# Performance work log

Hardware: AMD Instinct MI355X
Metric: run time of the kernel (lower is better)

## Reference

```python
import jax, jax.numpy as jnp
import numpy as np

HEADS = 16
NEG_INF = np.float32(-2**32 + 1)  # matches TF code's padding value


def setup_inputs() -> dict:
    key = jax.random.key(0)
    ks = jax.random.split(key, 11)
    B, S, D = 2, 2048, 1024
    mk = lambda k, shape: jax.random.normal(k, shape, dtype=jnp.float32)
    return {
        "query": mk(ks[0], (B, S, D)),
        "key":   mk(ks[1], (B, S, D)),
        "value": mk(ks[2], (B, S, D)),
        "Wq": mk(ks[3], (D, D)) * (1.0 / np.sqrt(D)), "bq": jnp.zeros((D,), jnp.float32),
        "Wk": mk(ks[4], (D, D)) * (1.0 / np.sqrt(D)), "bk": jnp.zeros((D,), jnp.float32),
        "Wv": mk(ks[5], (D, D)) * (1.0 / np.sqrt(D)), "bv": jnp.zeros((D,), jnp.float32),
        "Wo": mk(ks[6], (D, D)) * (1.0 / np.sqrt(D)), "bo": jnp.zeros((D,), jnp.float32),
    }


def reference(query, key, value, Wq, bq, Wk, bk, Wv, bv, Wo, bo):
    B, S, D = query.shape
    H = HEADS
    dh = D // H
    # QKV projections with relu (as in the original Dense(activation=relu))
    q = jax.nn.relu(query @ Wq + bq).reshape(B, S, H, dh)
    k = jax.nn.relu(key   @ Wk + bk).reshape(B, S, H, dh)
    v = jax.nn.relu(value @ Wv + bv).reshape(B, S, H, dh)
    # scaled dot-product attention; scale = sqrt(per-head key dim)
    scores = jnp.einsum("bqhd,bkhd->bhqk", q, k) / jnp.sqrt(jnp.float32(dh))
    # causal mask (masked=True path): zeros above the diagonal -> NEG_INF
    causal = jnp.tril(jnp.ones((S, S), dtype=jnp.float32))  # [S,S]
    scores = jnp.where(causal == 0, NEG_INF, scores)
    attn = jax.nn.softmax(scores, axis=-1)  # [B,H,S,S]
    out = jnp.einsum("bhqk,bkhd->bqhd", attn, v).reshape(B, S, D)
    return jax.nn.relu(out @ Wo + bo)
```

## Files before the change

### kernel.cpp

```cpp
#include <hip/hip_runtime.h>
#include <hip/hip_bf16.h>

using bf16 = __hip_bfloat16;
typedef __attribute__((ext_vector_type(8))) short bf16x8;
typedef __attribute__((ext_vector_type(4))) float f32x4;

#define DEV __device__ __forceinline__

DEV void gload_lds16(const void* g, void* l) {
  __builtin_amdgcn_global_load_lds((const __attribute__((address_space(1))) void*)g,
                                   (__attribute__((address_space(3))) void*)l, 16, 0, 0);
}

DEV unsigned pk2(float lo, float hi) {
  union { bf16 h[2]; unsigned u; } z;
  z.h[0] = __float2bfloat16(lo);
  z.h[1] = __float2bfloat16(hi);
  return z.u;
}

struct PrepArgs {
  const float* x[3]; bf16* y[3];
  const float* W[4]; bf16* WT[4];
};

__global__ __launch_bounds__(256) void prep_kernel(PrepArgs a) {
  __shared__ float tile[32][33];
  const int b = blockIdx.x;
  if (b < 6144) {
    const int which = b >> 11, blk = b & 2047;
    const int i = blk * 256 + threadIdx.x;
    const float4* xv = (const float4*)a.x[which];
    float4 p = xv[i * 2];
    float4 q = xv[i * 2 + 1];
    union { bf16 h[8]; uint4 v; } u;
    u.h[0] = __float2bfloat16(p.x); u.h[1] = __float2bfloat16(p.y);
    u.h[2] = __float2bfloat16(p.z); u.h[3] = __float2bfloat16(p.w);
    u.h[4] = __float2bfloat16(q.x); u.h[5] = __float2bfloat16(q.y);
    u.h[6] = __float2bfloat16(q.z); u.h[7] = __float2bfloat16(q.w);
    *(uint4*)&a.y[which][(size_t)i * 8] = u.v;
  } else {
    const int w = (b - 6144) >> 10, blk = (b - 6144) & 1023;
    const float* W = a.W[w];
    bf16* WT = a.WT[w];
    const int tx = threadIdx.x & 31, ty = threadIdx.x >> 5;
    const int n0 = (blk & 31) * 32, k0 = (blk >> 5) * 32;
#pragma unroll
    for (int i = ty; i < 32; i += 8)
      tile[i][tx] = W[(size_t)(k0 + i) * 1024 + n0 + tx];
    __syncthreads();
#pragma unroll
    for (int i = ty; i < 32; i += 8)
      WT[(size_t)(n0 + i) * 1024 + k0 + tx] = __float2bfloat16(tile[tx][i]);
  }
}

__global__ __launch_bounds__(256) void vtrans_kernel(const bf16* __restrict__ v,
                                                     bf16* __restrict__ VT) {
  __shared__ bf16 tile[64 * 64];
  const int t = threadIdx.x;
  const int bh = blockIdx.y, b = bh >> 4, h = bh & 15;
  const int s0 = blockIdx.x * 64;
  const int r0 = t >> 3, c8 = t & 7;
#pragma unroll
  for (int it = 0; it < 2; ++it) {
    int r = it * 32 + r0;
    uint4 d = *(const uint4*)&v[(size_t)(b * 2048 + s0 + r) * 1024 + h * 64 + c8 * 8];
    *(uint4*)&tile[r * 64 + ((c8 ^ (r >> 3)) * 8)] = d;
  }
  __syncthreads();
#pragma unroll
  for (int it = 0; it < 2; ++it) {
    int d = it * 32 + r0;
    int sc = c8 * 8;
    union { bf16 h[8]; uint4 v4; } u;
#pragma unroll
    for (int j = 0; j < 8; ++j) {
      int row = sc + j;
      u.h[j] = tile[row * 64 + (((d >> 3) ^ (row >> 3)) * 8) + (d & 7)];
    }
    *(uint4*)&VT[((size_t)bh * 64 + d) * 2048 + s0 + sc] = u.v4;
  }
}

template <typename OutT>
DEV void gemm128_core(const bf16* __restrict__ A, const bf16* __restrict__ BT,
                      const float* __restrict__ bias, OutT* __restrict__ out) {
  constexpr int K = 1024, N = 1024;
  __shared__ bf16 ldsA[2][128 * 32];
  __shared__ bf16 ldsB[2][128 * 32];
  const int t = threadIdx.x;
  const int lane = t & 63, wid = t >> 6;
  const int wr = wid >> 1, wc = wid & 1;
  const int fr = lane & 15, fko = (lane >> 4) * 8;
  const size_t mBase = (size_t)blockIdx.y * 128;
  const size_t nBase = (size_t)blockIdx.x * 128;

  const int srow = t >> 2;
  const int scol = (t & 3) * 8;
  const bf16* gA = A + (mBase + srow) * K + scol;
  const bf16* gB = BT + (nBase + srow) * K + scol;
  const int ldst = wid * 512;

  f32x4 acc[4][4];
#pragma unroll
  for (int i = 0; i < 4; ++i)
#pragma unroll
    for (int j = 0; j < 4; ++j) acc[i][j] = (f32x4){0.f, 0.f, 0.f, 0.f};

  gload_lds16(gA, &ldsA[0][ldst]);
  gload_lds16(gA + 64 * K, &ldsA[0][ldst + 2048]);
  gload_lds16(gB, &ldsB[0][ldst]);
  gload_lds16(gB + 64 * K, &ldsB[0][ldst + 2048]);
  __syncthreads();

  int buf = 0;
  for (int k0 = 0; k0 < K; k0 += 32) {
    if (k0 + 32 < K) {
      const int kn = k0 + 32;
      gload_lds16(gA + kn, &ldsA[buf ^ 1][ldst]);
      gload_lds16(gA + 64 * K + kn, &ldsA[buf ^ 1][ldst + 2048]);
      gload_lds16(gB + kn, &ldsB[buf ^ 1][ldst]);
      gload_lds16(gB + 64 * K + kn, &ldsB[buf ^ 1][ldst + 2048]);
    }
    bf16x8 aF[4], bF[4];
#pragma unroll
    for (int i = 0; i < 4; ++i)
      aF[i] = *(const bf16x8*)&ldsA[buf][(wr * 64 + i * 16 + fr) * 32 + fko];
#pragma unroll
    for (int j = 0; j < 4; ++j)
      bF[j] = *(const bf16x8*)&ldsB[buf][(wc * 64 + j * 16 + fr) * 32 + fko];
#pragma unroll
    for (int i = 0; i < 4; ++i)
#pragma unroll
      for (int j = 0; j < 4; ++j)
        acc[i][j] = __builtin_amdgcn_mfma_f32_16x16x32_bf16(aF[i], bF[j], acc[i][j], 0, 0, 0);
    __syncthreads();
    buf ^= 1;
  }

  const int orow = (int)mBase + wr * 64 + (lane >> 4) * 4;
  const int ocol = (int)nBase + wc * 64 + fr;
#pragma unroll
  for (int j = 0; j < 4; ++j) {
    const float bj = bias[ocol + j * 16];
#pragma unroll
    for (int i = 0; i < 4; ++i)
#pragma unroll
      for (int r = 0; r < 4; ++r) {
        float v = fmaxf(acc[i][j][r] + bj, 0.f);
        size_t idx = (size_t)(orow + i * 16 + r) * N + (ocol + j * 16);
        if constexpr (sizeof(OutT) == 2) out[idx] = __float2bfloat16(v);
        else out[idx] = v;
      }
  }
}

struct QKVArgs {
  const bf16* A[3];
  const bf16* BT[3];
  const float* bias[3];
  bf16* out[3];
};

__global__ __launch_bounds__(256) void gemm_qkv_kernel(QKVArgs args) {
  const int z = blockIdx.z;
  gemm128_core<bf16>(args.A[z], args.BT[z], args.bias[z], args.out[z]);
}

__global__ __launch_bounds__(256) void gemm_out_kernel(const bf16* __restrict__ A,
                                                       const bf16* __restrict__ BT,
                                                       const float* __restrict__ bias,
                                                       float* __restrict__ out) {
  gemm128_core<float>(A, BT, bias, out);
}

__global__ __launch_bounds__(256, 4) void attn_kernel(const bf16* __restrict__ Qb,
                                                      const bf16* __restrict__ Kb,
                                                      const bf16* __restrict__ VTb,
                                                      bf16* __restrict__ Ob) {
  constexpr int Dm = 1024, S = 2048;
  __shared__ bf16 ldsKV[16384];
  const int t = threadIdx.x, l = t & 63, wid = t >> 6;

  const int lin = blockIdx.y * 16 + blockIdx.x;
  const int swz = (lin & 7) * 64 + (lin >> 3);
  const int bh = swz >> 4, pairp = swz & 15;
  const int b = bh >> 4, h = bh & 15;
  const int q4 = l & 15, fg = l >> 4;
  const bf16* Qg = Qb + (size_t)b * S * Dm + h * 64;
  const bf16* Kg = Kb + (size_t)b * S * Dm + h * 64;
  const bf16* VTg = VTb + (size_t)bh * 64 * S;

  const int srow = l >> 3;
  const int schunk = (l & 7) ^ srow;
  const bf16* kSrc = Kg + (size_t)(wid * 16 + srow) * Dm + schunk * 8;
  const bf16* vSrc = VTg + (size_t)(wid * 16 + srow) * S + schunk * 8;
  bf16* kDst = ldsKV + wid * 1024;
  bf16* vDst = ldsKV + 8192 + wid * 1024;

  const int idx0 = ((q4 + ((l & 16) ? 32 : 0)) << 2);
  const int idx1 = idx0 + 64;

#pragma unroll 1
  for (int ph = 0; ph < 2; ++ph) {
    const int qt = ph ? (31 - pairp) : pairp;
    const int qb = qt * 64;
    const int qw = qb + wid * 16;

    bf16x8 qF[2];
#pragma unroll
    for (int kd = 0; kd < 2; ++kd)
      qF[kd] = *(const bf16x8*)&Qg[(size_t)(qw + q4) * Dm + kd * 32 + fg * 8];

    f32x4 oacc[4];
#pragma unroll
    for (int n = 0; n < 4; ++n) oacc[n] = (f32x4){0.f, 0.f, 0.f, 0.f};
    float mrow = -3.0e38f, lsum = 0.f;

    const int nTiles = qt + 1;

    gload_lds16(kSrc, kDst);
    gload_lds16(kSrc + 8 * Dm, kDst + 512);
    gload_lds16(vSrc, vDst);
    gload_lds16(vSrc + 8 * S, vDst + 512);
    __syncthreads();

    int buf = 0;
    for (int tile = 0; tile < nTiles; ++tile) {
      const int kvb = tile * 64;
      if (tile + 1 < nTiles) {
        const int nb = kvb + 64;
        gload_lds16(kSrc + (size_t)nb * Dm, kDst + (buf ^ 1) * 4096);
        gload_lds16(kSrc + (size_t)(nb + 8) * Dm, kDst + (buf ^ 1) * 4096 + 512);
        gload_lds16(vSrc + nb, vDst + (buf ^ 1) * 4096);
        gload_lds16(vSrc + nb + 8 * S, vDst + (buf ^ 1) * 4096 + 512);
      }
      const bf16* kb = ldsKV + buf * 4096;
      const bf16* vb = ldsKV + 8192 + buf * 4096;

      f32x4 sT[4];
#pragma unroll
      for (int n = 0; n < 4; ++n) sT[n] = (f32x4){0.f, 0.f, 0.f, 0.f};
      __builtin_amdgcn_s_setprio(1);
#pragma unroll
      for (int n = 0; n < 4; ++n) {
#pragma unroll
        for (int kd = 0; kd < 2; ++kd) {
          bf16x8 kf = *(const bf16x8*)&kb[(n * 16 + q4) * 64 + (((kd * 4 + fg) ^ (q4 & 7)) * 8)];
          sT[n] = __builtin_amdgcn_mfma_f32_16x16x32_bf16(kf, qF[kd], sT[n], 0, 0, 0);
        }
      }
      __builtin_amdgcn_s_setprio(0);
      const bool needmask = (tile == nTiles - 1);
      const int qrow = qw + q4;
#pragma unroll
      for (int n = 0; n < 4; ++n)
#pragma unroll
        for (int r = 0; r < 4; ++r) {
          float vv = sT[n][r] * 0.125f;
          if (needmask) {
            int kv = kvb + n * 16 + fg * 4 + r;
            if (kv > qrow) vv = -1e30f;
          }
          sT[n][r] = vv;
        }
      float tmax = -3.0e38f;
#pragma unroll
      for (int n = 0; n < 4; ++n)
        tmax = fmaxf(tmax, fmaxf(fmaxf(sT[n][0], sT[n][1]), fmaxf(sT[n][2], sT[n][3])));
      tmax = fmaxf(tmax, __shfl_xor(tmax, 16, 64));
      tmax = fmaxf(tmax, __shfl_xor(tmax, 32, 64));
      const float mnew = fmaxf(mrow, tmax);
      const float corr = __expf(mrow - mnew);
      mrow = mnew;
      float rs = 0.f;
#pragma unroll
      for (int n = 0; n < 4; ++n)
#pragma unroll
        for (int r = 0; r < 4; ++r) {
          float p = __expf(sT[n][r] - mnew);
          sT[n][r] = p;
          rs += p;
        }
      rs += __shfl_xor(rs, 16, 64);
      rs += __shfl_xor(rs, 32, 64);
      lsum = lsum * corr + rs;
#pragma unroll
      for (int n = 0; n < 4; ++n)
#pragma unroll
        for (int r = 0; r < 4; ++r) oacc[n][r] *= corr;

#pragma unroll
      for (int ks = 0; ks < 2; ++ks) {
        const unsigned X0 = pk2(sT[2 * ks][0], sT[2 * ks][1]);
        const unsigned X1 = pk2(sT[2 * ks][2], sT[2 * ks][3]);
        const unsigned Y0 = pk2(sT[2 * ks + 1][0], sT[2 * ks + 1][1]);
        const unsigned Y1 = pk2(sT[2 * ks + 1][2], sT[2 * ks + 1][3]);
        union { int u[4]; bf16x8 v; } bfr;
        {
          int zx = __builtin_amdgcn_ds_bpermute(idx0, (int)X0);
          int zy = __builtin_amdgcn_ds_bpermute(idx0, (int)Y0);
          bfr.u[0] = (l & 32) ? zy : zx;
          zx = __builtin_amdgcn_ds_bpermute(idx0, (int)X1);
          zy = __builtin_amdgcn_ds_bpermute(idx0, (int)Y1);
          bfr.u[1] = (l & 32) ? zy : zx;
          zx = __builtin_amdgcn_ds_bpermute(idx1, (int)X0);
          zy = __builtin_amdgcn_ds_bpermute(idx1, (int)Y0);
          bfr.u[2] = (l & 32) ? zy : zx;
          zx = __builtin_amdgcn_ds_bpermute(idx1, (int)X1);
          zy = __builtin_amdgcn_ds_bpermute(idx1, (int)Y1);
          bfr.u[3] = (l & 32) ? zy : zx;
        }
        __builtin_amdgcn_s_setprio(1);
#pragma unroll
        for (int dblk = 0; dblk < 4; ++dblk) {
          bf16x8 vf = *(const bf16x8*)&vb[(dblk * 16 + q4) * 64 + (((ks * 4 + fg) ^ (q4 & 7)) * 8)];
          oacc[dblk] = __builtin_amdgcn_mfma_f32_16x16x32_bf16(vf, bfr.v, oacc[dblk], 0, 0, 0);
        }
        __builtin_amdgcn_s_setprio(0);
      }
      __syncthreads();
      buf ^= 1;
    }

    bf16* ldsT = ldsKV + wid * 1152;
    const float inv = 1.f / lsum;
#pragma unroll
    for (int dblk = 0; dblk < 4; ++dblk)
#pragma unroll
      for (int r = 0; r < 4; ++r) {
        int d = dblk * 16 + fg * 4 + r;
        ldsT[q4 * 72 + d] = __float2bfloat16(oacc[dblk][r] * inv);
      }
    asm volatile("s_waitcnt lgkmcnt(0)" ::: "memory");
    __builtin_amdgcn_sched_barrier(0);
    const int rq = l >> 2, dq = (l & 3) * 16;
#pragma unroll
    for (int i = 0; i < 2; ++i) {
      uint4 w = *(const uint4*)&ldsT[rq * 72 + dq + 8 * i];
      *(uint4*)&Ob[((size_t)b * S + qw + rq) * Dm + h * 64 + dq + 8 * i] = w;
    }
    __syncthreads();
  }
}

extern "C" void kernel_launch(void* const* d_in, const int* in_sizes, int n_in,
                              void* d_out, int out_size, void* d_ws, size_t ws_size,
                              hipStream_t stream) {
  const float* query = (const float*)d_in[0];
  const float* key   = (const float*)d_in[1];
  const float* value = (const float*)d_in[2];
  const float* Wq = (const float*)d_in[3]; const float* bq = (const float*)d_in[4];
  const float* Wk = (const float*)d_in[5]; const float* bk = (const float*)d_in[6];
  const float* Wv = (const float*)d_in[7]; const float* bv = (const float*)d_in[8];
  const float* Wo = (const float*)d_in[9]; const float* bo = (const float*)d_in[10];
  float* out = (float*)d_out;

  char* ws = (char*)d_ws;
  const size_t MB = 1024 * 1024;
  bf16* xq  = (bf16*)(ws + 0 * MB);
  bf16* xk  = (bf16*)(ws + 8 * MB);
  bf16* xv  = (bf16*)(ws + 16 * MB);
  bf16* qp  = (bf16*)(ws + 24 * MB);
  bf16* kp  = (bf16*)(ws + 32 * MB);
  bf16* vp  = (bf16*)(ws + 40 * MB);
  bf16* WqT = (bf16*)(ws + 48 * MB);
  bf16* WkT = (bf16*)(ws + 50 * MB);
  bf16* WvT = (bf16*)(ws + 52 * MB);
  bf16* WoT = (bf16*)(ws + 54 * MB);
  bf16* VT   = xq;
  bf16* attn = xk;

  PrepArgs pa;
  pa.x[0] = query; pa.x[1] = key; pa.x[2] = value;
  pa.y[0] = xq; pa.y[1] = xk; pa.y[2] = xv;
  pa.W[0] = Wq; pa.W[1] = Wk; pa.W[2] = Wv; pa.W[3] = Wo;
  pa.WT[0] = WqT; pa.WT[1] = WkT; pa.WT[2] = WvT; pa.WT[3] = WoT;
  prep_kernel<<<10240, 256, 0, stream>>>(pa);

  QKVArgs qa;
  qa.A[0] = xq;  qa.A[1] = xk;  qa.A[2] = xv;
  qa.BT[0] = WqT; qa.BT[1] = WkT; qa.BT[2] = WvT;
  qa.bias[0] = bq; qa.bias[1] = bk; qa.bias[2] = bv;
  qa.out[0] = qp; qa.out[1] = kp; qa.out[2] = vp;
  gemm_qkv_kernel<<<dim3(8, 32, 3), 256, 0, stream>>>(qa);

  vtrans_kernel<<<dim3(32, 32), 256, 0, stream>>>(vp, VT);
  attn_kernel<<<dim3(16, 32), 256, 0, stream>>>(qp, kp, VT, attn);
  gemm_out_kernel<<<dim3(8, 32), 256, 0, stream>>>(attn, WoT, bo, out);
}
```

Baseline: 233.7 us.

## Widen attention KV tiles to 128, use exp2 with lazy rescale, shrink out-GEMM tile

The attention kernel now stages 128-row K/V tiles instead of 64, with a new swizzled layout and double buffering. It switches softmax to exp2 with the log2e factor folded into the scale, and rescales the running output only when the row max grows by more than a threshold. The output projection GEMM uses 64-row M tiles, doubling its grid to improve occupancy across CUs. The larger LDS footprint reduces attention occupancy to 2 blocks, and the coarser causal tiling does some extra masked work on the diagonal.

```diff
diff --git a/kernel.cpp b/kernel.cpp
--- a/kernel.cpp
+++ b/kernel.cpp
@@ -6,6 +6,8 @@
 typedef __attribute__((ext_vector_type(4))) float f32x4;
 
 #define DEV __device__ __forceinline__
+
+DEV float exp2fast(float x) { return __builtin_amdgcn_exp2f(x); }
 
 DEV void gload_lds16(const void* g, void* l) {
   __builtin_amdgcn_global_load_lds((const __attribute__((address_space(1))) void*)g,
@@ -83,17 +85,18 @@
   }
 }
 
-template <typename OutT>
-DEV void gemm128_core(const bf16* __restrict__ A, const bf16* __restrict__ BT,
-                      const float* __restrict__ bias, OutT* __restrict__ out) {
+template <int BM, typename OutT>
+DEV void gemm_core(const bf16* __restrict__ A, const bf16* __restrict__ BT,
+                   const float* __restrict__ bias, OutT* __restrict__ out) {
   constexpr int K = 1024, N = 1024;
-  __shared__ bf16 ldsA[2][128 * 32];
+  constexpr int MI = BM / 32;
+  __shared__ bf16 ldsA[2][BM * 32];
   __shared__ bf16 ldsB[2][128 * 32];
   const int t = threadIdx.x;
   const int lane = t & 63, wid = t >> 6;
   const int wr = wid >> 1, wc = wid & 1;
   const int fr = lane & 15, fko = (lane >> 4) * 8;
-  const size_t mBase = (size_t)blockIdx.y * 128;
+  const size_t mBase = (size_t)blockIdx.y * BM;
   const size_t nBase = (size_t)blockIdx.x * 128;
 
   const int srow = t >> 2;
@@ -102,14 +105,14 @@
   const bf16* gB = BT + (nBase + srow) * K + scol;
   const int ldst = wid * 512;
 
-  f32x4 acc[4][4];
-#pragma unroll
-  for (int i = 0; i < 4; ++i)
+  f32x4 acc[MI][4];
+#pragma unroll
+  for (int i = 0; i < MI; ++i)
 #pragma unroll
     for (int j = 0; j < 4; ++j) acc[i][j] = (f32x4){0.f, 0.f, 0.f, 0.f};
 
   gload_lds16(gA, &ldsA[0][ldst]);
-  gload_lds16(gA + 64 * K, &ldsA[0][ldst + 2048]);
+  if constexpr (BM == 128) gload_lds16(gA + 64 * K, &ldsA[0][ldst + 2048]);
   gload_lds16(gB, &ldsB[0][ldst]);
   gload_lds16(gB + 64 * K, &ldsB[0][ldst + 2048]);
   __syncthreads();
@@ -119,19 +122,19 @@
     if (k0 + 32 < K) {
       const int kn = k0 + 32;
       gload_lds16(gA + kn, &ldsA[buf ^ 1][ldst]);
-      gload_lds16(gA + 64 * K + kn, &ldsA[buf ^ 1][ldst + 2048]);
+      if constexpr (BM == 128) gload_lds16(gA + 64 * K + kn, &ldsA[buf ^ 1][ldst + 2048]);
       gload_lds16(gB + kn, &ldsB[buf ^ 1][ldst]);
       gload_lds16(gB + 64 * K + kn, &ldsB[buf ^ 1][ldst + 2048]);
     }
-    bf16x8 aF[4], bF[4];
-#pragma unroll
-    for (int i = 0; i < 4; ++i)
-      aF[i] = *(const bf16x8*)&ldsA[buf][(wr * 64 + i * 16 + fr) * 32 + fko];
+    bf16x8 aF[MI], bF[4];
+#pragma unroll
+    for (int i = 0; i < MI; ++i)
+      aF[i] = *(const bf16x8*)&ldsA[buf][(wr * (BM / 2) + i * 16 + fr) * 32 + fko];
 #pragma unroll
     for (int j = 0; j < 4; ++j)
       bF[j] = *(const bf16x8*)&ldsB[buf][(wc * 64 + j * 16 + fr) * 32 + fko];
 #pragma unroll
-    for (int i = 0; i < 4; ++i)
+    for (int i = 0; i < MI; ++i)
 #pragma unroll
       for (int j = 0; j < 4; ++j)
         acc[i][j] = __builtin_amdgcn_mfma_f32_16x16x32_bf16(aF[i], bF[j], acc[i][j], 0, 0, 0);
@@ -139,13 +142,13 @@
     buf ^= 1;
   }
 
-  const int orow = (int)mBase + wr * 64 + (lane >> 4) * 4;
+  const int orow = (int)mBase + wr * (BM / 2) + (lane >> 4) * 4;
   const int ocol = (int)nBase + wc * 64 + fr;
 #pragma unroll
   for (int j = 0; j < 4; ++j) {
     const float bj = bias[ocol + j * 16];
 #pragma unroll
-    for (int i = 0; i < 4; ++i)
+    for (int i = 0; i < MI; ++i)
 #pragma unroll
       for (int r = 0; r < 4; ++r) {
         float v = fmaxf(acc[i][j][r] + bj, 0.f);
@@ -165,22 +168,23 @@
 
 __global__ __launch_bounds__(256) void gemm_qkv_kernel(QKVArgs args) {
   const int z = blockIdx.z;
-  gemm128_core<bf16>(args.A[z], args.BT[z], args.bias[z], args.out[z]);
+  gemm_core<128, bf16>(args.A[z], args.BT[z], args.bias[z], args.out[z]);
 }
 
 __global__ __launch_bounds__(256) void gemm_out_kernel(const bf16* __restrict__ A,
                                                        const bf16* __restrict__ BT,
                                                        const float* __restrict__ bias,
                                                        float* __restrict__ out) {
-  gemm128_core<float>(A, BT, bias, out);
-}
-
-__global__ __launch_bounds__(256, 4) void attn_kernel(const bf16* __restrict__ Qb,
+  gemm_core<64, float>(A, BT, bias, out);
+}
+
+__global__ __launch_bounds__(256, 2) void attn_kernel(const bf16* __restrict__ Qb,
                                                       const bf16* __restrict__ Kb,
                                                       const bf16* __restrict__ VTb,
                                                       bf16* __restrict__ Ob) {
   constexpr int Dm = 1024, S = 2048;
-  __shared__ bf16 ldsKV[16384];
+  __shared__ bf16 ldsK[2][128 * 64];
+  __shared__ bf16 ldsV[2][64 * 128];
   const int t = threadIdx.x, l = t & 63, wid = t >> 6;
 
   const int lin = blockIdx.y * 16 + blockIdx.x;
@@ -192,15 +196,30 @@
   const bf16* Kg = Kb + (size_t)b * S * Dm + h * 64;
   const bf16* VTg = VTb + (size_t)bh * 64 * S;
 
-  const int srow = l >> 3;
-  const int schunk = (l & 7) ^ srow;
-  const bf16* kSrc = Kg + (size_t)(wid * 16 + srow) * Dm + schunk * 8;
-  const bf16* vSrc = VTg + (size_t)(wid * 16 + srow) * S + schunk * 8;
-  bf16* kDst = ldsKV + wid * 1024;
-  bf16* vDst = ldsKV + 8192 + wid * 1024;
+  const int krow0 = wid * 32 + (l >> 3);
+  const int kch = ((l & 7) ^ (l >> 3)) * 8;
+  const int vrl = l >> 4;
+  const int vcb = l & 15;
 
   const int idx0 = ((q4 + ((l & 16) ? 32 : 0)) << 2);
   const int idx1 = idx0 + 64;
+
+  constexpr float SC = 0.18033688f;
+
+  auto STAGE = [&](int tile, int bi) {
+    const int kvb = tile * 128;
+#pragma unroll
+    for (int g = 0; g < 4; ++g)
+      gload_lds16(Kg + (size_t)(kvb + krow0 + 8 * g) * Dm + kch,
+                  &ldsK[bi][(wid * 32 + 8 * g) * 64]);
+#pragma unroll
+    for (int g = 0; g < 4; ++g) {
+      const int dr = wid * 16 + 4 * g + vrl;
+      const int vch = (vcb ^ (4 * g + vrl)) * 8;
+      gload_lds16(VTg + (size_t)dr * S + kvb + vch,
+                  &ldsV[bi][(wid * 16 + 4 * g) * 128]);
+    }
+  };
 
 #pragma unroll 1
   for (int ph = 0; ph < 2; ++ph) {
@@ -218,33 +237,24 @@
     for (int n = 0; n < 4; ++n) oacc[n] = (f32x4){0.f, 0.f, 0.f, 0.f};
     float mrow = -3.0e38f, lsum = 0.f;
 
-    const int nTiles = qt + 1;
-
-    gload_lds16(kSrc, kDst);
-    gload_lds16(kSrc + 8 * Dm, kDst + 512);
-    gload_lds16(vSrc, vDst);
-    gload_lds16(vSrc + 8 * S, vDst + 512);
+    const int nTiles = (qt + 2) >> 1;
+
+    STAGE(0, 0);
     __syncthreads();
 
     int buf = 0;
     for (int tile = 0; tile < nTiles; ++tile) {
-      const int kvb = tile * 64;
-      if (tile + 1 < nTiles) {
-        const int nb = kvb + 64;
-        gload_lds16(kSrc + (size_t)nb * Dm, kDst + (buf ^ 1) * 4096);
-        gload_lds16(kSrc + (size_t)(nb + 8) * Dm, kDst + (buf ^ 1) * 4096 + 512);
-        gload_lds16(vSrc + nb, vDst + (buf ^ 1) * 4096);
-        gload_lds16(vSrc + nb + 8 * S, vDst + (buf ^ 1) * 4096 + 512);
-      }
-      const bf16* kb = ldsKV + buf * 4096;
-      const bf16* vb = ldsKV + 8192 + buf * 4096;
-
-      f32x4 sT[4];
-#pragma unroll
-      for (int n = 0; n < 4; ++n) sT[n] = (f32x4){0.f, 0.f, 0.f, 0.f};
+      const int kvb = tile * 128;
+      if (tile + 1 < nTiles) STAGE(tile + 1, buf ^ 1);
+      const bf16* kb = &ldsK[buf][0];
+      const bf16* vb = &ldsV[buf][0];
+
+      f32x4 sT[8];
+#pragma unroll
+      for (int n = 0; n < 8; ++n) sT[n] = (f32x4){0.f, 0.f, 0.f, 0.f};
       __builtin_amdgcn_s_setprio(1);
 #pragma unroll
-      for (int n = 0; n < 4; ++n) {
+      for (int n = 0; n < 8; ++n) {
 #pragma unroll
         for (int kd = 0; kd < 2; ++kd) {
           bf16x8 kf = *(const bf16x8*)&kb[(n * 16 + q4) * 64 + (((kd * 4 + fg) ^ (q4 & 7)) * 8)];
@@ -252,70 +262,74 @@
         }
       }
       __builtin_amdgcn_s_setprio(0);
+
       const bool needmask = (tile == nTiles - 1);
       const int qrow = qw + q4;
 #pragma unroll
-      for (int n = 0; n < 4; ++n)
+      for (int n = 0; n < 8; ++n)
 #pragma unroll
         for (int r = 0; r < 4; ++r) {
-          float vv = sT[n][r] * 0.125f;
+          float vv = sT[n][r] * SC;
           if (needmask) {
             int kv = kvb + n * 16 + fg * 4 + r;
             if (kv > qrow) vv = -1e30f;
           }
           sT[n][r] = vv;
         }
-      float tmax = -3.0e38f;
-#pragma unroll
-      for (int n = 0; n < 4; ++n)
-        tmax = fmaxf(tmax, fmaxf(fmaxf(sT[n][0], sT[n][1]), fmaxf(sT[n][2], sT[n][3])));
+      float vm[8];
+#pragma unroll
+      for (int n = 0; n < 8; ++n)
+        vm[n] = fmaxf(fmaxf(sT[n][0], sT[n][1]), fmaxf(sT[n][2], sT[n][3]));
+      float tmax = fmaxf(fmaxf(fmaxf(vm[0], vm[1]), fmaxf(vm[2], vm[3])),
+                         fmaxf(fmaxf(vm[4], vm[5]), fmaxf(vm[6], vm[7])));
       tmax = fmaxf(tmax, __shfl_xor(tmax, 16, 64));
       tmax = fmaxf(tmax, __shfl_xor(tmax, 32, 64));
-      const float mnew = fmaxf(mrow, tmax);
-      const float corr = __expf(mrow - mnew);
-      mrow = mnew;
-      float rs = 0.f;
-#pragma unroll
-      for (int n = 0; n < 4; ++n)
-#pragma unroll
-        for (int r = 0; r < 4; ++r) {
-          float p = __expf(sT[n][r] - mnew);
-          sT[n][r] = p;
-          rs += p;
-        }
+      if (__any(tmax > mrow + 8.f)) {
+        const float mnew = fmaxf(mrow, tmax);
+        const float corr = exp2fast(mrow - mnew);
+        mrow = mnew;
+        lsum *= corr;
+#pragma unroll
+        for (int n = 0; n < 4; ++n)
+#pragma unroll
+          for (int r = 0; r < 4; ++r) oacc[n][r] *= corr;
+      }
+      float rv[8];
+#pragma unroll
+      for (int n = 0; n < 8; ++n) {
+#pragma unroll
+        for (int r = 0; r < 4; ++r) sT[n][r] = exp2fast(sT[n][r] - mrow);
+        rv[n] = (sT[n][0] + sT[n][1]) + (sT[n][2] + sT[n][3]);
+      }
+      float rs = ((rv[0] + rv[1]) + (rv[2] + rv[3])) + ((rv[4] + rv[5]) + (rv[6] + rv[7]));
       rs += __shfl_xor(rs, 16, 64);
       rs += __shfl_xor(rs, 32, 64);
-      lsum = lsum * corr + rs;
-#pragma unroll
-      for (int n = 0; n < 4; ++n)
-#pragma unroll
-        for (int r = 0; r < 4; ++r) oacc[n][r] *= corr;
-
-#pragma unroll
-      for (int ks = 0; ks < 2; ++ks) {
+      lsum += rs;
+
+#pragma unroll
+      for (int ks = 0; ks < 4; ++ks) {
         const unsigned X0 = pk2(sT[2 * ks][0], sT[2 * ks][1]);
         const unsigned X1 = pk2(sT[2 * ks][2], sT[2 * ks][3]);
         const unsigned Y0 = pk2(sT[2 * ks + 1][0], sT[2 * ks + 1][1]);
         const unsigned Y1 = pk2(sT[2 * ks + 1][2], sT[2 * ks + 1][3]);
         union { int u[4]; bf16x8 v; } bfr;
-        {
-          int zx = __builtin_amdgcn_ds_bpermute(idx0, (int)X0);
-          int zy = __builtin_amdgcn_ds_bpermute(idx0, (int)Y0);
-          bfr.u[0] = (l & 32) ? zy : zx;
-          zx = __builtin_amdgcn_ds_bpermute(idx0, (int)X1);
-          zy = __builtin_amdgcn_ds_bpermute(idx0, (int)Y1);
-          bfr.u[1] = (l & 32) ? zy : zx;
-          zx = __builtin_amdgcn_ds_bpermute(idx1, (int)X0);
-          zy = __builtin_amdgcn_ds_bpermute(idx1, (int)Y0);
-          bfr.u[2] = (l & 32) ? zy : zx;
-          zx = __builtin_amdgcn_ds_bpermute(idx1, (int)X1);
-          zy = __builtin_amdgcn_ds_bpermute(idx1, (int)Y1);
-          bfr.u[3] = (l & 32) ? zy : zx;
-        }
+        int zx, zy;
+        zx = __builtin_amdgcn_ds_bpermute(idx0, (int)X0);
+        zy = __builtin_amdgcn_ds_bpermute(idx0, (int)Y0);
+        bfr.u[0] = (l & 32) ? zy : zx;
+        zx = __builtin_amdgcn_ds_bpermute(idx0, (int)X1);
+        zy = __builtin_amdgcn_ds_bpermute(idx0, (int)Y1);
+        bfr.u[1] = (l & 32) ? zy : zx;
+        zx = __builtin_amdgcn_ds_bpermute(idx1, (int)X0);
+        zy = __builtin_amdgcn_ds_bpermute(idx1, (int)Y0);
+        bfr.u[2] = (l & 32) ? zy : zx;
+        zx = __builtin_amdgcn_ds_bpermute(idx1, (int)X1);
+        zy = __builtin_amdgcn_ds_bpermute(idx1, (int)Y1);
+        bfr.u[3] = (l & 32) ? zy : zx;
         __builtin_amdgcn_s_setprio(1);
 #pragma unroll
         for (int dblk = 0; dblk < 4; ++dblk) {
-          bf16x8 vf = *(const bf16x8*)&vb[(dblk * 16 + q4) * 64 + (((ks * 4 + fg) ^ (q4 & 7)) * 8)];
+          bf16x8 vf = *(const bf16x8*)&vb[(dblk * 16 + q4) * 128 + (((ks * 4 + fg) ^ q4) * 8)];
           oacc[dblk] = __builtin_amdgcn_mfma_f32_16x16x32_bf16(vf, bfr.v, oacc[dblk], 0, 0, 0);
         }
         __builtin_amdgcn_s_setprio(0);
@@ -324,7 +338,7 @@
       buf ^= 1;
     }
 
-    bf16* ldsT = ldsKV + wid * 1152;
+    bf16* ldsT = &ldsK[0][0] + wid * 1152;
     const float inv = 1.f / lsum;
 #pragma unroll
     for (int dblk = 0; dblk < 4; ++dblk)
@@ -388,5 +402,5 @@
 
   vtrans_kernel<<<dim3(32, 32), 256, 0, stream>>>(vp, VT);
   attn_kernel<<<dim3(16, 32), 256, 0, stream>>>(qp, kp, VT, attn);
-  gemm_out_kernel<<<dim3(8, 32), 256, 0, stream>>>(attn, WoT, bo, out);
-}
+  gemm_out_kernel<<<dim3(8, 64), 256, 0, stream>>>(attn, WoT, bo, out);
+}
```

Result: no change. 235.9 us (+1.0%).
